# Optimization experiments

Hardware: AMD Instinct MI355X
Metric: run time of the kernel (lower is better)

The kernel has to match this reference:

```python
import jax, jax.numpy as jnp
import numpy as np

FLOAT_MIN = np.float32(np.finfo(np.float32).min)  # torch.finfo().min for float32
K_DIM = 64  # init kwarg, equals head dim of query/key


def setup_inputs() -> dict:
    key = jax.random.key(0)
    k1, k2, k3, k4 = jax.random.split(key, 4)
    B, Lq, Lk, D, Dv = 16, 2048, 2048, 64, 64
    return {
        "query": jax.random.normal(k1, (B, Lq, D), dtype=jnp.float32),
        "key": jax.random.normal(k2, (B, Lk, D), dtype=jnp.float32),
        "value": jax.random.normal(k3, (B, Lk, Dv), dtype=jnp.float32),
        "mask": jax.random.uniform(k4, (1, Lq, Lk), dtype=jnp.float32),
    }


def reference(query, key, value, mask):
    # scores: [B, Lq, Lk]
    scores = jnp.einsum("bqd,bkd->bqk", query, key) / jnp.sqrt(jnp.float32(K_DIM))
    # multiplicative mask -> additive log-bias, clamped at float32 min
    scores = scores + jnp.maximum(jnp.log(mask), FLOAT_MIN)
    # NOTE: source applies softmax over dim=1 (the query axis), faithfully reproduced
    attn = jax.nn.softmax(scores, axis=1)
    return jnp.einsum("bqk,bkv->bqv", attn, value)
```

## Files before the change

kernel.cpp:

```cpp
#include <hip/hip_runtime.h>
#include <cstdint>
#include <cstddef>


#define LSEQ 2048
#define DHEAD 64

typedef __bf16 v8bf __attribute__((ext_vector_type(8)));
typedef __bf16 v4bf __attribute__((ext_vector_type(4)));
typedef float v4f __attribute__((ext_vector_type(4)));

#define MFMA16(a, b, c) __builtin_amdgcn_mfma_f32_16x16x32_bf16(a, b, c, 0, 0, 0)

__device__ __forceinline__ void gl_lds16(const void* g, void* l) {
  __builtin_amdgcn_global_load_lds(
      (__attribute__((address_space(1))) void*)g,
      (__attribute__((address_space(3))) void*)l, 16, 0, 0);
}

__global__ __launch_bounds__(256) void cast_qk(const float* __restrict__ Q,
                                               const float* __restrict__ K,
                                               __bf16* __restrict__ Qb,
                                               __bf16* __restrict__ Kb,
                                               float* __restrict__ outz,
                                               float* __restrict__ Lz) {
  size_t j = (size_t)blockIdx.x * 256 + threadIdx.x;
  size_t i = j * 4;
  float4 q = *(const float4*)(Q + i);
  float4 k = *(const float4*)(K + i);
  v4bf qo = {(__bf16)(q.x * 0.125f), (__bf16)(q.y * 0.125f),
             (__bf16)(q.z * 0.125f), (__bf16)(q.w * 0.125f)};
  v4bf ko = {(__bf16)k.x, (__bf16)k.y, (__bf16)k.z, (__bf16)k.w};
  *(v4bf*)(Qb + i) = qo;
  *(v4bf*)(Kb + i) = ko;
  float4 z = {0.f, 0.f, 0.f, 0.f};
  *(float4*)(outz + i) = z;
  if (j < (size_t)16 * LSEQ) Lz[j] = 0.f;
}

__global__ __launch_bounds__(256, 3) void stats_k(const __bf16* __restrict__ Qb,
                                                  const __bf16* __restrict__ Kb,
                                                  const float* __restrict__ mask,
                                                  float* __restrict__ Lsum) {
  const int bx = blockIdx.x;
  const int b = bx >> 6;
  const int qc = (bx >> 4) & 3;
  const int k0 = (bx & 15) * 128;
  const int tid = threadIdx.x;
  const int w = tid >> 6, lane = tid & 63;
  const int quad = lane >> 4, n = lane & 15;

  __shared__ __align__(16) __bf16 Qt[2][64 * 64];
  __shared__ float psum[4][128];

#define STAGE_Q(buf, q0s)                                                        \
  {                                                                              \
    _Pragma("unroll") for (int i = 0; i < 2; ++i) {                              \
      int s = (w * 2 + i) * 64 + lane;                                           \
      int row = s >> 3, gc = (s & 7) ^ (row & 7);                                \
      gl_lds16(Qb + ((size_t)b * LSEQ + (q0s) + row) * DHEAD + gc * 8,           \
               &Qt[buf][s * 8]);                                                 \
    }                                                                            \
  }

  v8bf ak[8][2];
#pragma unroll
  for (int sub = 0; sub < 8; ++sub)
#pragma unroll
    for (int dh = 0; dh < 2; ++dh)
      ak[sub][dh] = *(const v8bf*)(Kb + ((size_t)b * LSEQ + k0 + sub * 16 + n) * DHEAD +
                                   dh * 32 + quad * 8);

  float csum[8][4];
#pragma unroll
  for (int sub = 0; sub < 8; ++sub)
#pragma unroll
    for (int r = 0; r < 4; ++r) csum[sub][r] = 0.f;

  const int qbeg = qc * 512;
  STAGE_Q(0, qbeg);
  __syncthreads();

  int cur = 0;
#pragma unroll 1
  for (int ks = 0; ks < 8; ++ks) {
    const int qs = qbeg + ks * 64;
    v4f m4[8];
#pragma unroll
    for (int sub = 0; sub < 8; ++sub)
      m4[sub] = *(const v4f*)(mask + (size_t)(qs + w * 16 + n) * LSEQ + k0 + sub * 16 +
                              quad * 4);
    if (ks < 7) STAGE_Q(cur ^ 1, qs + 64);

    const int qr = w * 16 + n;
    v8bf bq[2];
#pragma unroll
    for (int dh = 0; dh < 2; ++dh)
      bq[dh] = *(const v8bf*)&Qt[cur][qr * 64 + ((dh * 4 + quad) ^ (qr & 7)) * 8];

#pragma unroll
    for (int sub = 0; sub < 8; ++sub) {
      v4f c = {0.f, 0.f, 0.f, 0.f};
      c = MFMA16(ak[sub][0], bq[0], c);
      c = MFMA16(ak[sub][1], bq[1], c);
#pragma unroll
      for (int r = 0; r < 4; ++r) csum[sub][r] += m4[sub][r] * __expf(c[r]);
    }
    __syncthreads();
    cur ^= 1;
  }
#undef STAGE_Q

#pragma unroll
  for (int sub = 0; sub < 8; ++sub)
#pragma unroll
    for (int r = 0; r < 4; ++r) {
      float v = csum[sub][r];
      v += __shfl_xor(v, 1);
      v += __shfl_xor(v, 2);
      v += __shfl_xor(v, 4);
      v += __shfl_xor(v, 8);
      if (n == 0) psum[w][sub * 16 + quad * 4 + r] = v;
    }
  __syncthreads();
  if (tid < 128) {
    float s = psum[0][tid] + psum[1][tid] + psum[2][tid] + psum[3][tid];
    unsafeAtomicAdd(&Lsum[(size_t)b * LSEQ + k0 + tid], s);
  }
}

__global__ __launch_bounds__(256) void vtrans_k(const float* __restrict__ V,
                                                const float* __restrict__ Lsum,
                                                __bf16* __restrict__ Vts) {
  const int b = blockIdx.x >> 6;
  const int k0 = (blockIdx.x & 63) * 32;
  const int tid = threadIdx.x;
  __shared__ float tile[32][65];
  __shared__ float invl[32];
  if (tid < 32) invl[tid] = 1.0f / Lsum[(size_t)b * LSEQ + k0 + tid];
#pragma unroll
  for (int t = 0; t < 8; ++t) {
    int flat = t * 256 + tid;
    int k = flat >> 6, v = flat & 63;
    tile[k][v] = V[((size_t)b * LSEQ + k0 + k) * DHEAD + v];
  }
  __syncthreads();
#pragma unroll
  for (int t = 0; t < 8; ++t) {
    int flat = t * 256 + tid;
    int v = flat >> 5, k = flat & 31;
    Vts[((size_t)b * DHEAD + v) * LSEQ + k0 + k] = (__bf16)(tile[k][v] * invl[k]);
  }
}

__global__ __launch_bounds__(256, 3) void attn_k(const __bf16* __restrict__ Qb,
                                                 const __bf16* __restrict__ Kb,
                                                 const __bf16* __restrict__ Vts,
                                                 const float* __restrict__ mask,
                                                 float* __restrict__ out) {
  const int bx = blockIdx.x;
  const int b = bx >> 6;
  const int kc = (bx >> 4) & 3;
  const int q0 = (bx & 15) * 128;
  const int tid = threadIdx.x;
  const int w = tid >> 6, lane = tid & 63;
  const int quad = lane >> 4, n = lane & 15;

  __shared__ __align__(16) __bf16 Kt[2][64 * 64];
  __shared__ __align__(16) __bf16 Vt[2][64 * 64];
  __shared__ __align__(16) __bf16 Pt[128][72];

#define STAGE_KV(buf, kb2)                                                       \
  {                                                                              \
    _Pragma("unroll") for (int i = 0; i < 2; ++i) {                              \
      int s = (w * 2 + i) * 64 + lane;                                           \
      int row = s >> 3, gc = (s & 7) ^ (row & 7);                                \
      gl_lds16(Kb + ((size_t)b * LSEQ + (kb2) + row) * DHEAD + gc * 8,           \
               &Kt[buf][s * 8]);                                                 \
      gl_lds16(Vts + ((size_t)b * DHEAD + row) * LSEQ + (kb2) + gc * 8,          \
               &Vt[buf][s * 8]);                                                 \
    }                                                                            \
  }

  const int qg0 = q0 + w * 32 + n;

  v8bf bq[2][2];
#pragma unroll
  for (int h = 0; h < 2; ++h)
#pragma unroll
    for (int dh = 0; dh < 2; ++dh)
      bq[h][dh] = *(const v8bf*)(Qb + ((size_t)b * LSEQ + qg0 + h * 16) * DHEAD +
                                 dh * 32 + quad * 8);

  v4f acc[2][4];
#pragma unroll
  for (int h = 0; h < 2; ++h)
#pragma unroll
    for (int vs = 0; vs < 4; ++vs) acc[h][vs] = (v4f){0.f, 0.f, 0.f, 0.f};

  const int kbeg = kc * 512;
  STAGE_KV(0, kbeg);
  __syncthreads();

  int cur = 0;
#pragma unroll 1
  for (int ks = 0; ks < 8; ++ks) {
    const int kb = kbeg + ks * 64;
    v4f m4[2][4];
#pragma unroll
    for (int h = 0; h < 2; ++h)
#pragma unroll
      for (int sub = 0; sub < 4; ++sub)
        m4[h][sub] = *(const v4f*)(mask + (size_t)(qg0 + h * 16) * LSEQ + kb + sub * 16 +
                                   quad * 4);
    if (ks < 7) STAGE_KV(cur ^ 1, kb + 64);

#pragma unroll
    for (int sub = 0; sub < 4; ++sub) {
      const int kr = sub * 16 + n;
      v8bf a0 = *(const v8bf*)&Kt[cur][kr * 64 + ((quad) ^ (kr & 7)) * 8];
      v8bf a1 = *(const v8bf*)&Kt[cur][kr * 64 + ((4 + quad) ^ (kr & 7)) * 8];
#pragma unroll
      for (int h = 0; h < 2; ++h) {
        v4f c = {0.f, 0.f, 0.f, 0.f};
        c = MFMA16(a0, bq[h][0], c);
        c = MFMA16(a1, bq[h][1], c);
        v4bf pv;
#pragma unroll
        for (int r = 0; r < 4; ++r) pv[r] = (__bf16)(m4[h][sub][r] * __expf(c[r]));
        *(v4bf*)&Pt[w * 32 + h * 16 + n][sub * 16 + quad * 4] = pv;
      }
    }
    __asm__ volatile("s_waitcnt lgkmcnt(0)" ::: "memory");

#pragma unroll
    for (int kk = 0; kk < 2; ++kk) {
      v8bf ap0 = *(const v8bf*)&Pt[w * 32 + n][kk * 32 + quad * 8];
      v8bf ap1 = *(const v8bf*)&Pt[w * 32 + 16 + n][kk * 32 + quad * 8];
#pragma unroll
      for (int vs = 0; vs < 4; ++vs) {
        const int vr = vs * 16 + n;
        v8bf bv = *(const v8bf*)&Vt[cur][vr * 64 + ((kk * 4 + quad) ^ (vr & 7)) * 8];
        acc[0][vs] = MFMA16(ap0, bv, acc[0][vs]);
        acc[1][vs] = MFMA16(ap1, bv, acc[1][vs]);
      }
    }
    __syncthreads();
    cur ^= 1;
  }
#undef STAGE_KV

#pragma unroll
  for (int h = 0; h < 2; ++h)
#pragma unroll
    for (int vs = 0; vs < 4; ++vs)
#pragma unroll
      for (int r = 0; r < 4; ++r)
        unsafeAtomicAdd(&out[((size_t)b * LSEQ + q0 + w * 32 + h * 16 + quad * 4 + r) *
                                 DHEAD +
                             vs * 16 + n],
                        acc[h][vs][r]);
}

extern "C" void kernel_launch(void* const* d_in, const int* in_sizes, int n_in,
                              void* d_out, int out_size, void* d_ws, size_t ws_size,
                              hipStream_t stream) {
  const float* Q = (const float*)d_in[0];
  const float* K = (const float*)d_in[1];
  const float* V = (const float*)d_in[2];
  const float* mask = (const float*)d_in[3];
  float* out = (float*)d_out;

  char* ws = (char*)d_ws;
  __bf16* Qb = (__bf16*)(ws);
  __bf16* Kb = (__bf16*)(ws + (4 << 20));
  __bf16* Vts = (__bf16*)(ws + (8 << 20));
  float* Lsum = (float*)(ws + (12 << 20));
  const size_t need = ((size_t)12 << 20) + (1 << 17);
  if (ws_size < need) return;

  cast_qk<<<2048, 256, 0, stream>>>(Q, K, Qb, Kb, out, Lsum);
  stats_k<<<1024, 256, 0, stream>>>(Qb, Kb, mask, Lsum);
  vtrans_k<<<1024, 256, 0, stream>>>(V, Lsum, Vts);
  attn_k<<<1024, 256, 0, stream>>>(Qb, Kb, Vts, mask, out);
}
```

Before: 190.8 us.

## Single-buffer K/V with split staging, swizzle P tile, shrink stats tiles, add setprio

In attn_k, the double-buffered K/V tiles become single buffers. K and V are now staged at separate points, each after the barrier that frees its buffer, and the padded P tile is replaced by an XOR-swizzled unpadded layout. Together these cut LDS use so occupancy can rise to 4 blocks per CU. stats_k halves its key tile per block (64 instead of 128) and doubles the grid, and both kernels wrap their MFMA sections in s_setprio. The trade-off is less load/compute overlap from single buffering plus an extra barrier per iteration, in exchange for higher occupancy and fewer LDS bank conflicts.

```diff
diff --git a/kernel.cpp b/kernel.cpp
--- a/kernel.cpp
+++ b/kernel.cpp
@@ -38,20 +38,20 @@
   if (j < (size_t)16 * LSEQ) Lz[j] = 0.f;
 }
 
-__global__ __launch_bounds__(256, 3) void stats_k(const __bf16* __restrict__ Qb,
+__global__ __launch_bounds__(256, 4) void stats_k(const __bf16* __restrict__ Qb,
                                                   const __bf16* __restrict__ Kb,
                                                   const float* __restrict__ mask,
                                                   float* __restrict__ Lsum) {
   const int bx = blockIdx.x;
-  const int b = bx >> 6;
-  const int qc = (bx >> 4) & 3;
-  const int k0 = (bx & 15) * 128;
+  const int b = bx >> 7;
+  const int qc = (bx >> 5) & 3;
+  const int k0 = (bx & 31) * 64;
   const int tid = threadIdx.x;
   const int w = tid >> 6, lane = tid & 63;
   const int quad = lane >> 4, n = lane & 15;
 
   __shared__ __align__(16) __bf16 Qt[2][64 * 64];
-  __shared__ float psum[4][128];
+  __shared__ float psum[4][64];
 
 #define STAGE_Q(buf, q0s)                                                        \
   {                                                                              \
@@ -63,17 +63,17 @@
     }                                                                            \
   }
 
-  v8bf ak[8][2];
-#pragma unroll
-  for (int sub = 0; sub < 8; ++sub)
+  v8bf ak[4][2];
+#pragma unroll
+  for (int sub = 0; sub < 4; ++sub)
 #pragma unroll
     for (int dh = 0; dh < 2; ++dh)
       ak[sub][dh] = *(const v8bf*)(Kb + ((size_t)b * LSEQ + k0 + sub * 16 + n) * DHEAD +
                                    dh * 32 + quad * 8);
 
-  float csum[8][4];
-#pragma unroll
-  for (int sub = 0; sub < 8; ++sub)
+  float csum[4][4];
+#pragma unroll
+  for (int sub = 0; sub < 4; ++sub)
 #pragma unroll
     for (int r = 0; r < 4; ++r) csum[sub][r] = 0.f;
 
@@ -85,9 +85,9 @@
 #pragma unroll 1
   for (int ks = 0; ks < 8; ++ks) {
     const int qs = qbeg + ks * 64;
-    v4f m4[8];
-#pragma unroll
-    for (int sub = 0; sub < 8; ++sub)
+    v4f m4[4];
+#pragma unroll
+    for (int sub = 0; sub < 4; ++sub)
       m4[sub] = *(const v4f*)(mask + (size_t)(qs + w * 16 + n) * LSEQ + k0 + sub * 16 +
                               quad * 4);
     if (ks < 7) STAGE_Q(cur ^ 1, qs + 64);
@@ -98,21 +98,23 @@
     for (int dh = 0; dh < 2; ++dh)
       bq[dh] = *(const v8bf*)&Qt[cur][qr * 64 + ((dh * 4 + quad) ^ (qr & 7)) * 8];
 
-#pragma unroll
-    for (int sub = 0; sub < 8; ++sub) {
+    __builtin_amdgcn_s_setprio(1);
+#pragma unroll
+    for (int sub = 0; sub < 4; ++sub) {
       v4f c = {0.f, 0.f, 0.f, 0.f};
       c = MFMA16(ak[sub][0], bq[0], c);
       c = MFMA16(ak[sub][1], bq[1], c);
 #pragma unroll
       for (int r = 0; r < 4; ++r) csum[sub][r] += m4[sub][r] * __expf(c[r]);
     }
+    __builtin_amdgcn_s_setprio(0);
     __syncthreads();
     cur ^= 1;
   }
 #undef STAGE_Q
 
 #pragma unroll
-  for (int sub = 0; sub < 8; ++sub)
+  for (int sub = 0; sub < 4; ++sub)
 #pragma unroll
     for (int r = 0; r < 4; ++r) {
       float v = csum[sub][r];
@@ -123,7 +125,7 @@
       if (n == 0) psum[w][sub * 16 + quad * 4 + r] = v;
     }
   __syncthreads();
-  if (tid < 128) {
+  if (tid < 64) {
     float s = psum[0][tid] + psum[1][tid] + psum[2][tid] + psum[3][tid];
     unsafeAtomicAdd(&Lsum[(size_t)b * LSEQ + k0 + tid], s);
   }
@@ -153,7 +155,7 @@
   }
 }
 
-__global__ __launch_bounds__(256, 3) void attn_k(const __bf16* __restrict__ Qb,
+__global__ __launch_bounds__(256, 4) void attn_k(const __bf16* __restrict__ Qb,
                                                  const __bf16* __restrict__ Kb,
                                                  const __bf16* __restrict__ Vts,
                                                  const float* __restrict__ mask,
@@ -166,19 +168,26 @@
   const int w = tid >> 6, lane = tid & 63;
   const int quad = lane >> 4, n = lane & 15;
 
-  __shared__ __align__(16) __bf16 Kt[2][64 * 64];
-  __shared__ __align__(16) __bf16 Vt[2][64 * 64];
-  __shared__ __align__(16) __bf16 Pt[128][72];
-
-#define STAGE_KV(buf, kb2)                                                       \
+  __shared__ __align__(16) __bf16 Kt[64 * 64];
+  __shared__ __align__(16) __bf16 Vt[64 * 64];
+  __shared__ __align__(16) __bf16 Pt[128 * 64];
+
+#define STAGE_K(kb2)                                                             \
   {                                                                              \
     _Pragma("unroll") for (int i = 0; i < 2; ++i) {                              \
       int s = (w * 2 + i) * 64 + lane;                                           \
       int row = s >> 3, gc = (s & 7) ^ (row & 7);                                \
       gl_lds16(Kb + ((size_t)b * LSEQ + (kb2) + row) * DHEAD + gc * 8,           \
-               &Kt[buf][s * 8]);                                                 \
+               &Kt[s * 8]);                                                      \
+    }                                                                            \
+  }
+#define STAGE_V(kb2)                                                             \
+  {                                                                              \
+    _Pragma("unroll") for (int i = 0; i < 2; ++i) {                              \
+      int s = (w * 2 + i) * 64 + lane;                                           \
+      int row = s >> 3, gc = (s & 7) ^ (row & 7);                                \
       gl_lds16(Vts + ((size_t)b * DHEAD + row) * LSEQ + (kb2) + gc * 8,          \
-               &Vt[buf][s * 8]);                                                 \
+               &Vt[s * 8]);                                                      \
     }                                                                            \
   }
 
@@ -199,10 +208,10 @@
     for (int vs = 0; vs < 4; ++vs) acc[h][vs] = (v4f){0.f, 0.f, 0.f, 0.f};
 
   const int kbeg = kc * 512;
-  STAGE_KV(0, kbeg);
+  STAGE_K(kbeg);
+  STAGE_V(kbeg);
   __syncthreads();
 
-  int cur = 0;
 #pragma unroll 1
   for (int ks = 0; ks < 8; ++ks) {
     const int kb = kbeg + ks * 64;
@@ -213,13 +222,13 @@
       for (int sub = 0; sub < 4; ++sub)
         m4[h][sub] = *(const v4f*)(mask + (size_t)(qg0 + h * 16) * LSEQ + kb + sub * 16 +
                                    quad * 4);
-    if (ks < 7) STAGE_KV(cur ^ 1, kb + 64);
-
+
+    __builtin_amdgcn_s_setprio(1);
 #pragma unroll
     for (int sub = 0; sub < 4; ++sub) {
       const int kr = sub * 16 + n;
-      v8bf a0 = *(const v8bf*)&Kt[cur][kr * 64 + ((quad) ^ (kr & 7)) * 8];
-      v8bf a1 = *(const v8bf*)&Kt[cur][kr * 64 + ((4 + quad) ^ (kr & 7)) * 8];
+      v8bf a0 = *(const v8bf*)&Kt[kr * 64 + ((quad) ^ (kr & 7)) * 8];
+      v8bf a1 = *(const v8bf*)&Kt[kr * 64 + ((4 + quad) ^ (kr & 7)) * 8];
 #pragma unroll
       for (int h = 0; h < 2; ++h) {
         v4f c = {0.f, 0.f, 0.f, 0.f};
@@ -228,27 +237,37 @@
         v4bf pv;
 #pragma unroll
         for (int r = 0; r < 4; ++r) pv[r] = (__bf16)(m4[h][sub][r] * __expf(c[r]));
-        *(v4bf*)&Pt[w * 32 + h * 16 + n][sub * 16 + quad * 4] = pv;
+        const int prow = w * 32 + h * 16 + n;
+        *(v4bf*)((char*)Pt + prow * 128 + (((sub * 2 + (quad >> 1)) ^ (n & 7)) << 4) +
+                 ((quad & 1) << 3)) = pv;
       }
     }
-    __asm__ volatile("s_waitcnt lgkmcnt(0)" ::: "memory");
-
+    __builtin_amdgcn_s_setprio(0);
+    __syncthreads();
+    if (ks < 7) STAGE_K(kb + 64);
+
+    __builtin_amdgcn_s_setprio(1);
 #pragma unroll
     for (int kk = 0; kk < 2; ++kk) {
-      v8bf ap0 = *(const v8bf*)&Pt[w * 32 + n][kk * 32 + quad * 8];
-      v8bf ap1 = *(const v8bf*)&Pt[w * 32 + 16 + n][kk * 32 + quad * 8];
+      const int pr0 = w * 32 + n, pr1 = pr0 + 16;
+      v8bf ap0 =
+          *(const v8bf*)((char*)Pt + pr0 * 128 + (((kk * 4 + quad) ^ (n & 7)) << 4));
+      v8bf ap1 =
+          *(const v8bf*)((char*)Pt + pr1 * 128 + (((kk * 4 + quad) ^ (n & 7)) << 4));
 #pragma unroll
       for (int vs = 0; vs < 4; ++vs) {
         const int vr = vs * 16 + n;
-        v8bf bv = *(const v8bf*)&Vt[cur][vr * 64 + ((kk * 4 + quad) ^ (vr & 7)) * 8];
+        v8bf bv = *(const v8bf*)&Vt[vr * 64 + ((kk * 4 + quad) ^ (vr & 7)) * 8];
         acc[0][vs] = MFMA16(ap0, bv, acc[0][vs]);
         acc[1][vs] = MFMA16(ap1, bv, acc[1][vs]);
       }
     }
+    __builtin_amdgcn_s_setprio(0);
     __syncthreads();
-    cur ^= 1;
-  }
-#undef STAGE_KV
+    if (ks < 7) STAGE_V(kb + 64);
+  }
+#undef STAGE_K
+#undef STAGE_V
 
 #pragma unroll
   for (int h = 0; h < 2; ++h)
@@ -280,7 +299,7 @@
   if (ws_size < need) return;
 
   cast_qk<<<2048, 256, 0, stream>>>(Q, K, Qb, Kb, out, Lsum);
-  stats_k<<<1024, 256, 0, stream>>>(Qb, Kb, mask, Lsum);
+  stats_k<<<2048, 256, 0, stream>>>(Qb, Kb, mask, Lsum);
   vtrans_k<<<1024, 256, 0, stream>>>(V, Lsum, Vts);
   attn_k<<<1024, 256, 0, stream>>>(Qb, Kb, Vts, mask, out);
 }
```

New measurement: 184.3 us. -3.4%, faster.
